# Optimization experiments

Measured on AMD Instinct MI355X. Metric: run time of the kernel, lower is better.

## Reference

```python
import jax, jax.numpy as jnp
import numpy as np
from jax import lax


def _make_inds(n):
    # Indices of the inner n x n grid inside the (n+2) x (n+2) channel grid
    # (matches the torch module, which assumes kk == 1).
    ci = np.arange(n * n, dtype=np.int64).reshape(n, n)
    ci = ci + 1 + np.arange(n, dtype=np.int64)[:, None] * 2
    ci = ci + n + 2
    return jnp.asarray(ci.reshape(-1))


def setup_inputs() -> dict:
    key = jax.random.key(0)
    k1, _ = jax.random.split(key)
    n, kk = 14, 1
    n_in = n + 2 * kk
    B, H, W = 32, 64, 64
    x = jax.random.normal(k1, (B, n_in * n_in, H, W), dtype=jnp.float32)
    weight = jnp.ones((1,), dtype=jnp.float32)
    return {"x": x, "weight": weight, "n": n, "kk": kk}


def reference(x, weight, n, kk):
    B, C, H, W = x.shape
    n_in = n + 2 * kk
    win = 2 * kk + 1
    inds = _make_inds(n)

    valid_x = x[:, inds]  # [B, n^2, H, W]

    # exp(detach(x) * weight): gradient is blocked through x here
    xexp = jnp.exp(lax.stop_gradient(x) * weight[0])  # [B, n_in^2, H, W]

    # Windowed channel-grid sum: instead of the dense 1x1 conv with a mostly
    # zero [n^2, n_in^2] weight, do a (2kk+1)x(2kk+1) sliding-window sum over
    # the channel grid directly.
    grid = xexp.reshape(B, n_in, n_in, H * W)
    sums = lax.reduce_window(grid, jnp.float32(0), lax.add,
                             (1, win, win, 1), (1, 1, 1, 1), "VALID")
    denom = sums.reshape(B, n * n, H, W)

    imp = xexp[:, inds] / denom
    return valid_x * imp
```

## Files before the change

kernel.cpp:

```cpp
#include <hip/hip_runtime.h>
#include <hip/hip_bf16.h>


#define NIN 16
#define NOUT 14
#define HW 4096

__global__ __launch_bounds__(256) void fc_kernel(
    const float* __restrict__ x,
    const float* __restrict__ wp,
    float* __restrict__ out)
{
    const float w = wp[0];
    const int hw = blockIdx.x * blockDim.x + threadIdx.x;
    const int i  = blockIdx.y;
    const int b  = blockIdx.z;

    const float* xb = x + ((size_t)(b * (NIN * NIN) + i * NIN)) * HW + hw;

    float cs[NIN];
    float num[NIN];

    #pragma unroll
    for (int c = 0; c < NIN; ++c) {
        float v = xb[(size_t)c * HW];
        cs[c] = __expf(v * w);
    }
    #pragma unroll
    for (int c = 0; c < NIN; ++c) {
        float v = xb[(size_t)(NIN + c) * HW];
        float e = __expf(v * w);
        cs[c] += e;
        num[c] = v * e;
    }
    #pragma unroll
    for (int c = 0; c < NIN; ++c) {
        float v = xb[(size_t)(2 * NIN + c) * HW];
        cs[c] += __expf(v * w);
    }

    float* ob = out + ((size_t)(b * (NOUT * NOUT) + i * NOUT)) * HW + hw;
    #pragma unroll
    for (int j = 0; j < NOUT; ++j) {
        float denom = cs[j] + cs[j + 1] + cs[j + 2];
        ob[(size_t)j * HW] = __fdividef(num[j + 1], denom);
    }
}

extern "C" void kernel_launch(void* const* d_in, const int* in_sizes, int n_in,
                              void* d_out, int out_size, void* d_ws, size_t ws_size,
                              hipStream_t stream) {
    const float* x  = (const float*)d_in[0];
    const float* wp = (const float*)d_in[1];
    float* out = (float*)d_out;

    dim3 block(256, 1, 1);
    dim3 grid(HW / 256, NOUT, 32);
    hipLaunchKernelGGL(fc_kernel, grid, block, 0, stream, x, wp, out);
}
```

Measured before the change: 48.79 us.

## Stage exp values in LDS per pixel tile to avoid triple row reads

Each block now handles all 256 channels for a 32-pixel tile of one batch. Every input is read and exponentiated once into shared memory, and the 3x3 window sums are then formed from LDS rather than re-reading three channel rows from global memory. Loads and stores use float2 vectors. The cost is 32KB of LDS per block, a barrier, and only 14 of 16 thread groups active in the output phase. Global accesses now cover 128-byte row segments per channel instead of full 1KB rows.

```diff
diff --git a/kernel.cpp b/kernel.cpp
--- a/kernel.cpp
+++ b/kernel.cpp
@@ -5,45 +5,63 @@
 #define NIN 16
 #define NOUT 14
 #define HW 4096
+#define PIX 32
+#define SLOTS (PIX / 2)
+
+typedef float f2 __attribute__((ext_vector_type(2)));
 
 __global__ __launch_bounds__(256) void fc_kernel(
     const float* __restrict__ x,
     const float* __restrict__ wp,
     float* __restrict__ out)
 {
+    __shared__ f2 elds[NIN * NIN * SLOTS];
+
     const float w = wp[0];
-    const int hw = blockIdx.x * blockDim.x + threadIdx.x;
-    const int i  = blockIdx.y;
-    const int b  = blockIdx.z;
+    const int tid  = threadIdx.x;
+    const int slot = tid & (SLOTS - 1);
+    const int cg   = tid >> 4;
+    const int hw0  = blockIdx.x * PIX;
+    const int b    = blockIdx.y;
 
-    const float* xb = x + ((size_t)(b * (NIN * NIN) + i * NIN)) * HW + hw;
+    const float* xb = x + ((size_t)b * (NIN * NIN)) * HW + hw0 + slot * 2;
 
-    float cs[NIN];
-    float num[NIN];
+    f2 num[NIN];
 
     #pragma unroll
-    for (int c = 0; c < NIN; ++c) {
-        float v = xb[(size_t)c * HW];
-        cs[c] = __expf(v * w);
-    }
-    #pragma unroll
-    for (int c = 0; c < NIN; ++c) {
-        float v = xb[(size_t)(NIN + c) * HW];
-        float e = __expf(v * w);
-        cs[c] += e;
-        num[c] = v * e;
-    }
-    #pragma unroll
-    for (int c = 0; c < NIN; ++c) {
-        float v = xb[(size_t)(2 * NIN + c) * HW];
-        cs[c] += __expf(v * w);
+    for (int p = 0; p < NIN; ++p) {
+        const int ch = p * NIN + cg;
+        f2 v = *(const f2*)(xb + (size_t)ch * HW);
+        f2 e;
+        e.x = __expf(v.x * w);
+        e.y = __expf(v.y * w);
+        elds[ch * SLOTS + slot] = e;
+        num[p] = v * e;
     }
 
-    float* ob = out + ((size_t)(b * (NOUT * NOUT) + i * NOUT)) * HW + hw;
-    #pragma unroll
-    for (int j = 0; j < NOUT; ++j) {
-        float denom = cs[j] + cs[j + 1] + cs[j + 2];
-        ob[(size_t)j * HW] = __fdividef(num[j + 1], denom);
+    __syncthreads();
+
+    if (cg >= 1 && cg <= NOUT) {
+        const int j = cg - 1;
+
+        f2 rs[NIN];
+        #pragma unroll
+        for (int r = 0; r < NIN; ++r) {
+            f2 a = elds[(r * NIN + cg - 1) * SLOTS + slot];
+            f2 bb = elds[(r * NIN + cg    ) * SLOTS + slot];
+            f2 c = elds[(r * NIN + cg + 1) * SLOTS + slot];
+            rs[r] = a + bb + c;
+        }
+
+        float* ob = out + ((size_t)b * (NOUT * NOUT) + j) * HW + hw0 + slot * 2;
+        #pragma unroll
+        for (int i = 0; i < NOUT; ++i) {
+            f2 s = rs[i] + rs[i + 1] + rs[i + 2];
+            f2 d;
+            d.x = __fdividef(num[i + 1].x, s.x);
+            d.y = __fdividef(num[i + 1].y, s.y);
+            *(f2*)(ob + (size_t)(i * NOUT) * HW) = d;
+        }
     }
 }
 
@@ -55,6 +73,6 @@
     float* out = (float*)d_out;
 
     dim3 block(256, 1, 1);
-    dim3 grid(HW / 256, NOUT, 32);
+    dim3 grid(HW / PIX, 32, 1);
     hipLaunchKernelGGL(fc_kernel, grid, block, 0, stream, x, wp, out);
 }
```

New measurement: 40.53 us. -16.9%, faster.
